# Kernel tuning notes

Hardware: AMD Instinct MI355X
Metric: run time of the kernel (lower is better)

## Reference

```python
import jax, jax.numpy as jnp
import numpy as np

EPS = 1e-8


def setup_inputs() -> dict:
    key = jax.random.key(0)
    ks = jax.random.split(key, 7)
    S, B, E, D, A = 2048, 32, 1024, 1024, 1024
    return {
        "decoder_state": jax.random.normal(ks[0], (B, D), jnp.float32),
        "encoder_states": jax.random.normal(ks[1], (S, B, E), jnp.float32),
        "noise": jax.random.normal(ks[2], (S, B), jnp.float32),
        "W_dec": jax.random.normal(ks[3], (D, A), jnp.float32) * (D ** -0.5),
        "W_enc": jax.random.normal(ks[4], (E, A), jnp.float32) * (E ** -0.5),
        "b": jax.random.normal(ks[5], (A,), jnp.float32) * 0.02,
        "v": jax.random.normal(ks[6], (A,), jnp.float32) * (A ** -0.5),
    }


def reference(decoder_state, encoder_states, noise, W_dec, W_enc, b, v):
    S, B, E = encoder_states.shape
    # Additive (Bahdanau) monotonic energy: e_sb = v . tanh(W_d s + W_e h + b)
    dec_proj = decoder_state @ W_dec                         # [B, A]
    enc_proj = jnp.einsum("sbe,ea->sba", encoder_states, W_enc)  # [S, B, A]
    energy = jnp.einsum("sba,a->sb", jnp.tanh(enc_proj + dec_proj[None] + b), v)
    # p_choose with pre-sigmoid Gaussian noise (noise_avg=0, noise_var=1)
    p_choose = jax.nn.sigmoid(energy + noise)                # [S, B]

    # previous_attention is None -> one-hot at source position 0
    prev_attn = jnp.zeros((S, B), p_choose.dtype).at[0].set(1.0)

    # exclusive cumprod of (1 - p) along src dim
    cp = jnp.cumprod(1.0 - p_choose, axis=0)
    cumprod_one_minus_p = jnp.concatenate(
        [jnp.ones((1, B), p_choose.dtype), cp[:-1]], axis=0)
    denom = jnp.clip(cumprod_one_minus_p, EPS, 1.0)
    alpha = p_choose * cumprod_one_minus_p * jnp.cumsum(prev_attn / denom, axis=0)

    # mass preservation (no padding mask): dump residual mass on last frame
    residual = 1.0 - jnp.clip(jnp.sum(alpha[:-1], axis=0), 0.0, 1.0)
    alpha = alpha.at[-1].set(residual)

    beta = alpha  # hard monotonic attention: beta == alpha
    weighted_context = jnp.einsum("sbe,sb->be", encoder_states, beta)  # [B, E]
    return weighted_context, alpha
```

## Files before the change

### kernel.cpp

```cpp
#include <hip/hip_runtime.h>
#include <hip/hip_fp16.h>

#define S_DIM 2048
#define B_DIM 32
#define E_DIM 1024
#define A_DIM 1024
#define D_DIM 1024
#define M_DIM (S_DIM * B_DIM)

typedef _Float16 f16x8 __attribute__((ext_vector_type(8)));
typedef _Float16 f16x4 __attribute__((ext_vector_type(4)));
typedef float f32x4 __attribute__((ext_vector_type(4)));

#define OFF_ENC 0ull
#define OFF_WT  134217728ull
#define OFF_DP  (OFF_WT + 2097152ull)
#define OFF_EN  (OFF_DP + 131072ull)

__device__ inline void load_lds16(const void* g, void* l) {
    __builtin_amdgcn_global_load_lds((const __attribute__((address_space(1))) void*)g,
                                     (__attribute__((address_space(3))) void*)l, 16, 0, 0);
}

__global__ void convert_enc_kernel(const float4* __restrict__ in, f16x4* __restrict__ out) {
    int idx = blockIdx.x * 256 + threadIdx.x;
    float4 f = in[idx];
    f16x4 o = { (_Float16)f.x, (_Float16)f.y, (_Float16)f.z, (_Float16)f.w };
    out[idx] = o;
}

__global__ void transpose_wenc_kernel(const float* __restrict__ W, _Float16* __restrict__ WT) {
    __shared__ _Float16 tile[32][33];
    int a0 = blockIdx.x * 32, e0 = blockIdx.y * 32;
    int tx = threadIdx.x & 31, ty = threadIdx.x >> 5;
    #pragma unroll
    for (int i = 0; i < 32; i += 8)
        tile[ty + i][tx] = (_Float16)W[(size_t)(e0 + ty + i) * A_DIM + a0 + tx];
    __syncthreads();
    #pragma unroll
    for (int i = 0; i < 32; i += 8)
        WT[(size_t)(a0 + ty + i) * E_DIM + e0 + tx] = tile[tx][ty + i];
}

__global__ void decproj_kernel(const float* __restrict__ dec, const float* __restrict__ Wd,
                               const float* __restrict__ bias, float* __restrict__ dp) {
    int a = blockIdx.x * 256 + threadIdx.x;
    int b = blockIdx.y;
    float acc = bias[a];
    const float* dr = dec + (size_t)b * D_DIM;
    const float* wcol = Wd + a;
    #pragma unroll 8
    for (int d = 0; d < D_DIM; ++d)
        acc += dr[d] * wcol[(size_t)d * A_DIM];
    dp[(size_t)b * A_DIM + a] = acc;
}

__global__ __launch_bounds__(512, 2)
void energy_gemm_kernel(const _Float16* __restrict__ Af, const _Float16* __restrict__ Bt,
                        const float* __restrict__ dp, const float* __restrict__ v,
                        float* __restrict__ energy) {
    __shared__ alignas(16) _Float16 Atile[2][256 * 64];
    __shared__ alignas(16) _Float16 Btile[2][256 * 64];

    const int tid = threadIdx.x;
    const int wid = tid >> 6;
    const int lane = tid & 63;
    const int quad = lane >> 4;
    const int l15 = lane & 15;
    const int l7 = l15 & 7;

    const int bid = blockIdx.x;
    const int xcd = bid & 7;
    const int local = bid >> 3;
    const int m0 = (xcd * 32 + (local >> 2)) * 256;
    const int n0 = (local & 3) * 256;

    const int wm = (wid >> 2) * 128;
    const int wn = (wid & 3) * 64;

    const int lr = lane >> 3;
    const int lcol = ((lane & 7) ^ lr) * 8;
    const int srow = wid * 8;
    const _Float16* Ag = Af + (size_t)(m0 + srow + lr) * E_DIM + lcol;
    const _Float16* Bg = Bt + (size_t)(n0 + srow + lr) * E_DIM + lcol;

#define STAGE(bufi, k0)                                                       \
    {                                                                         \
        _Float16* ad = &Atile[bufi][srow * 64];                               \
        _Float16* bd = &Btile[bufi][srow * 64];                               \
        _Pragma("unroll")                                                     \
        for (int p = 0; p < 4; ++p) {                                         \
            load_lds16(Ag + (size_t)p * 64 * E_DIM + (k0), ad + p * 4096);    \
            load_lds16(Bg + (size_t)p * 64 * E_DIM + (k0), bd + p * 4096);    \
        }                                                                     \
    }

    f32x4 acc[8][4] = {};

    STAGE(0, 0)
    STAGE(1, 64)

    for (int t = 0; t < 16; ++t) {
        const int buf = t & 1;
        if (t == 15) asm volatile("s_waitcnt vmcnt(0)" ::: "memory");
        else         asm volatile("s_waitcnt vmcnt(8)" ::: "memory");
        __builtin_amdgcn_s_barrier();
        asm volatile("" ::: "memory");

        #pragma unroll
        for (int kh = 0; kh < 2; ++kh) {
            f16x8 bf[4];
            #pragma unroll
            for (int j = 0; j < 4; ++j) {
                const int row = wn + j * 16 + l15;
                const int slot = (quad + kh * 4) ^ l7;
                bf[j] = *(const f16x8*)&Btile[buf][row * 64 + slot * 8];
            }
            #pragma unroll
            for (int mh = 0; mh < 2; ++mh) {
                f16x8 af[4];
                #pragma unroll
                for (int i = 0; i < 4; ++i) {
                    const int row = wm + mh * 64 + i * 16 + l15;
                    const int slot = (quad + kh * 4) ^ l7;
                    af[i] = *(const f16x8*)&Atile[buf][row * 64 + slot * 8];
                }
                __builtin_amdgcn_s_setprio(1);
                #pragma unroll
                for (int i = 0; i < 4; ++i)
                    #pragma unroll
                    for (int j = 0; j < 4; ++j)
                        acc[mh * 4 + i][j] = __builtin_amdgcn_mfma_f32_16x16x32_f16(
                            af[i], bf[j], acc[mh * 4 + i][j], 0, 0, 0);
                __builtin_amdgcn_s_setprio(0);
            }
        }

        asm volatile("" ::: "memory");
        __builtin_amdgcn_s_barrier();
        asm volatile("" ::: "memory");
        if (t + 2 < 16) STAGE(buf, (t + 2) * 64)
    }
#undef STAGE

    float vf[4];
    #pragma unroll
    for (int j = 0; j < 4; ++j) vf[j] = v[n0 + wn + j * 16 + l15];

    #pragma unroll
    for (int i = 0; i < 8; ++i) {
        #pragma unroll
        for (int r = 0; r < 4; ++r) {
            int m = m0 + wm + i * 16 + quad * 4 + r;
            int bidx = m & 31;
            float sum = 0.f;
            #pragma unroll
            for (int j = 0; j < 4; ++j) {
                int a = n0 + wn + j * 16 + l15;
                float x = acc[i][j][r] + dp[bidx * A_DIM + a];
                float ex = __expf(2.f * x);
                float th = 1.f - 2.f * __builtin_amdgcn_rcpf(ex + 1.f);
                sum += th * vf[j];
            }
            sum += __shfl_xor(sum, 1);
            sum += __shfl_xor(sum, 2);
            sum += __shfl_xor(sum, 4);
            sum += __shfl_xor(sum, 8);
            if (l15 == 0) atomicAdd(&energy[bidx * S_DIM + (m >> 5)], sum);
        }
    }
}

__global__ void scan_alpha_kernel(const float* __restrict__ energy, const float* __restrict__ noise,
                                  float* __restrict__ alpha) {
    __shared__ float sc[256];
    __shared__ float red[256];
    const int b = blockIdx.x;
    const int t = threadIdx.x;
    float p[8], q[8];
    float prod = 1.f;
    #pragma unroll
    for (int k = 0; k < 8; ++k) {
        int s = t * 8 + k;
        float x = energy[b * S_DIM + s] + noise[s * B_DIM + b];
        p[k] = __builtin_amdgcn_rcpf(1.f + __expf(-x));
        q[k] = __builtin_amdgcn_rcpf(1.f + __expf(x));
        prod *= q[k];
    }
    sc[t] = prod;
    __syncthreads();
    for (int off = 1; off < 256; off <<= 1) {
        float mine = sc[t];
        float other = (t >= off) ? sc[t - off] : 1.f;
        __syncthreads();
        sc[t] = mine * other;
        __syncthreads();
    }
    float run = (t > 0) ? sc[t - 1] : 1.f;
    float lsum = 0.f;
    #pragma unroll
    for (int k = 0; k < 8; ++k) {
        int s = t * 8 + k;
        float al = p[k] * run;
        run *= q[k];
        if (s < S_DIM - 1) { alpha[s * B_DIM + b] = al; lsum += al; }
    }
    red[t] = lsum;
    __syncthreads();
    for (int off = 128; off > 0; off >>= 1) {
        if (t < off) red[t] += red[t + off];
        __syncthreads();
    }
    if (t == 0) {
        float tot = fminf(fmaxf(red[0], 0.f), 1.f);
        alpha[(S_DIM - 1) * B_DIM + b] = 1.f - tot;
    }
}

__global__ void wc_kernel(const _Float16* __restrict__ enc, const float* __restrict__ alpha,
                          float* __restrict__ wc) {
    __shared__ float red[128][8];
    const int b = blockIdx.y;
    const int t = threadIdx.x;
    const int e0 = (t & 127) * 8;
    const int half = t >> 7;
    int s = blockIdx.x * 128 + half;
    float acc[8] = {};
    for (int i = 0; i < 64; ++i, s += 2) {
        float al = alpha[s * B_DIM + b];
        f16x8 r = *(const f16x8*)&enc[((size_t)s * B_DIM + b) * E_DIM + e0];
        #pragma unroll
        for (int k = 0; k < 8; ++k) acc[k] += al * (float)r[k];
    }
    if (half) {
        #pragma unroll
        for (int k = 0; k < 8; ++k) red[t - 128][k] = acc[k];
    }
    __syncthreads();
    if (!half) {
        #pragma unroll
        for (int k = 0; k < 8; ++k)
            atomicAdd(&wc[b * E_DIM + e0 + k], acc[k] + red[t][k]);
    }
}

extern "C" void kernel_launch(void* const* d_in, const int* in_sizes, int n_in,
                              void* d_out, int out_size, void* d_ws, size_t ws_size,
                              hipStream_t stream) {
    const float* dec   = (const float*)d_in[0];
    const float* enc   = (const float*)d_in[1];
    const float* noise = (const float*)d_in[2];
    const float* Wd    = (const float*)d_in[3];
    const float* We    = (const float*)d_in[4];
    const float* bias  = (const float*)d_in[5];
    const float* v     = (const float*)d_in[6];

    char* ws = (char*)d_ws;
    _Float16* encf = (_Float16*)(ws + OFF_ENC);
    _Float16* wtf  = (_Float16*)(ws + OFF_WT);
    float* dp      = (float*)(ws + OFF_DP);
    float* energy  = (float*)(ws + OFF_EN);

    float* wc    = (float*)d_out;
    float* alpha = (float*)d_out + B_DIM * E_DIM;

    (void)hipMemsetAsync(wc, 0, B_DIM * E_DIM * sizeof(float), stream);
    (void)hipMemsetAsync(energy, 0, M_DIM * sizeof(float), stream);

    convert_enc_kernel<<<dim3(M_DIM * E_DIM / 4 / 256), 256, 0, stream>>>((const float4*)enc, (f16x4*)encf);
    transpose_wenc_kernel<<<dim3(32, 32), 256, 0, stream>>>(We, wtf);
    decproj_kernel<<<dim3(4, 32), 256, 0, stream>>>(dec, Wd, bias, dp);
    energy_gemm_kernel<<<dim3(1024), 512, 0, stream>>>(encf, wtf, dp, v, energy);
    scan_alpha_kernel<<<dim3(32), 256, 0, stream>>>(energy, noise, alpha);
    wc_kernel<<<dim3(16, 32), 256, 0, stream>>>(encf, alpha, wc);
}
```

Baseline: 678.9 us.

## Restructure energy GEMM main loop into 4-stage BK=32 pipeline with split A/B staging

```diff
diff --git a/kernel.cpp b/kernel.cpp
--- a/kernel.cpp
+++ b/kernel.cpp
@@ -59,15 +59,14 @@
 void energy_gemm_kernel(const _Float16* __restrict__ Af, const _Float16* __restrict__ Bt,
                         const float* __restrict__ dp, const float* __restrict__ v,
                         float* __restrict__ energy) {
-    __shared__ alignas(16) _Float16 Atile[2][256 * 64];
-    __shared__ alignas(16) _Float16 Btile[2][256 * 64];
+    __shared__ alignas(16) _Float16 As[4][256 * 32];
+    __shared__ alignas(16) _Float16 Bs[4][256 * 32];
 
     const int tid = threadIdx.x;
     const int wid = tid >> 6;
     const int lane = tid & 63;
     const int quad = lane >> 4;
     const int l15 = lane & 15;
-    const int l7 = l15 & 7;
 
     const int bid = blockIdx.x;
     const int xcd = bid & 7;
@@ -78,70 +77,82 @@
     const int wm = (wid >> 2) * 128;
     const int wn = (wid & 3) * 64;
 
-    const int lr = lane >> 3;
-    const int lcol = ((lane & 7) ^ lr) * 8;
-    const int srow = wid * 8;
-    const _Float16* Ag = Af + (size_t)(m0 + srow + lr) * E_DIM + lcol;
-    const _Float16* Bg = Bt + (size_t)(n0 + srow + lr) * E_DIM + lcol;
-
-#define STAGE(bufi, k0)                                                       \
-    {                                                                         \
-        _Float16* ad = &Atile[bufi][srow * 64];                               \
-        _Float16* bd = &Btile[bufi][srow * 64];                               \
-        _Pragma("unroll")                                                     \
-        for (int p = 0; p < 4; ++p) {                                         \
-            load_lds16(Ag + (size_t)p * 64 * E_DIM + (k0), ad + p * 4096);    \
-            load_lds16(Bg + (size_t)p * 64 * E_DIM + (k0), bd + p * 4096);    \
-        }                                                                     \
+    const int lr = lane >> 2;
+    const int lc = (lane & 3) * 8;
+    const _Float16* Ag = Af + (size_t)(m0 + wid * 16 + lr) * E_DIM + lc;
+    const _Float16* Bg = Bt + (size_t)(n0 + wid * 16 + lr) * E_DIM + lc;
+
+#define STAGE_A(u)                                                              \
+    {                                                                           \
+        load_lds16(Ag + (size_t)(u) * 32, &As[(u) & 3][wid * 512]);             \
+        load_lds16(Ag + (size_t)128 * E_DIM + (size_t)(u) * 32,                 \
+                   &As[(u) & 3][(wid + 8) * 512]);                              \
+    }
+#define STAGE_B(u)                                                              \
+    {                                                                           \
+        load_lds16(Bg + (size_t)(u) * 32, &Bs[(u) & 3][wid * 512]);             \
+        load_lds16(Bg + (size_t)128 * E_DIM + (size_t)(u) * 32,                 \
+                   &Bs[(u) & 3][(wid + 8) * 512]);                              \
     }
 
     f32x4 acc[8][4] = {};
 
-    STAGE(0, 0)
-    STAGE(1, 64)
-
-    for (int t = 0; t < 16; ++t) {
-        const int buf = t & 1;
-        if (t == 15) asm volatile("s_waitcnt vmcnt(0)" ::: "memory");
-        else         asm volatile("s_waitcnt vmcnt(8)" ::: "memory");
-        __builtin_amdgcn_s_barrier();
-        asm volatile("" ::: "memory");
-
-        #pragma unroll
-        for (int kh = 0; kh < 2; ++kh) {
-            f16x8 bf[4];
+    STAGE_A(0) STAGE_B(0)
+    STAGE_A(1) STAGE_B(1)
+    STAGE_A(2) STAGE_B(2)
+    asm volatile("s_waitcnt vmcnt(8)" ::: "memory");
+    __builtin_amdgcn_s_barrier();
+    asm volatile("" ::: "memory");
+
+    #pragma unroll
+    for (int t = 0; t < 32; ++t) {
+        const int slot = t & 3;
+        f16x8 af[4], bf[4];
+
+        #pragma unroll
+        for (int j = 0; j < 4; ++j)
+            bf[j] = *(const f16x8*)&Bs[slot][(wn + j * 16 + l15) * 32 + quad * 8];
+        #pragma unroll
+        for (int i = 0; i < 4; ++i)
+            af[i] = *(const f16x8*)&As[slot][(wm + i * 16 + l15) * 32 + quad * 8];
+        if (t < 29) STAGE_A(t + 3)
+        asm volatile("" ::: "memory");
+        __builtin_amdgcn_s_barrier();
+        asm volatile("" ::: "memory");
+        __builtin_amdgcn_s_setprio(1);
+        #pragma unroll
+        for (int i = 0; i < 4; ++i)
             #pragma unroll
-            for (int j = 0; j < 4; ++j) {
-                const int row = wn + j * 16 + l15;
-                const int slot = (quad + kh * 4) ^ l7;
-                bf[j] = *(const f16x8*)&Btile[buf][row * 64 + slot * 8];
-            }
+            for (int j = 0; j < 4; ++j)
+                acc[i][j] = __builtin_amdgcn_mfma_f32_16x16x32_f16(af[i], bf[j], acc[i][j], 0, 0, 0);
+        __builtin_amdgcn_s_setprio(0);
+        asm volatile("" ::: "memory");
+        __builtin_amdgcn_s_barrier();
+        asm volatile("" ::: "memory");
+
+        #pragma unroll
+        for (int i = 0; i < 4; ++i)
+            af[i] = *(const f16x8*)&As[slot][(wm + 64 + i * 16 + l15) * 32 + quad * 8];
+        if (t < 29) STAGE_B(t + 3)
+        asm volatile("" ::: "memory");
+        __builtin_amdgcn_s_barrier();
+        asm volatile("" ::: "memory");
+        __builtin_amdgcn_s_setprio(1);
+        #pragma unroll
+        for (int i = 0; i < 4; ++i)
             #pragma unroll
-            for (int mh = 0; mh < 2; ++mh) {
-                f16x8 af[4];
-                #pragma unroll
-                for (int i = 0; i < 4; ++i) {
-                    const int row = wm + mh * 64 + i * 16 + l15;
-                    const int slot = (quad + kh * 4) ^ l7;
-                    af[i] = *(const f16x8*)&Atile[buf][row * 64 + slot * 8];
-                }
-                __builtin_amdgcn_s_setprio(1);
-                #pragma unroll
-                for (int i = 0; i < 4; ++i)
-                    #pragma unroll
-                    for (int j = 0; j < 4; ++j)
-                        acc[mh * 4 + i][j] = __builtin_amdgcn_mfma_f32_16x16x32_f16(
-                            af[i], bf[j], acc[mh * 4 + i][j], 0, 0, 0);
-                __builtin_amdgcn_s_setprio(0);
-            }
-        }
-
-        asm volatile("" ::: "memory");
-        __builtin_amdgcn_s_barrier();
-        asm volatile("" ::: "memory");
-        if (t + 2 < 16) STAGE(buf, (t + 2) * 64)
-    }
-#undef STAGE
+            for (int j = 0; j < 4; ++j)
+                acc[4 + i][j] = __builtin_amdgcn_mfma_f32_16x16x32_f16(af[i], bf[j], acc[4 + i][j], 0, 0, 0);
+        __builtin_amdgcn_s_setprio(0);
+        if (t <= 28)      asm volatile("s_waitcnt vmcnt(8)" ::: "memory");
+        else if (t == 29) asm volatile("s_waitcnt vmcnt(4)" ::: "memory");
+        else if (t == 30) asm volatile("s_waitcnt vmcnt(0)" ::: "memory");
+        asm volatile("" ::: "memory");
+        __builtin_amdgcn_s_barrier();
+        asm volatile("" ::: "memory");
+    }
+#undef STAGE_A
+#undef STAGE_B
 
     float vf[4];
     #pragma unroll
```

Result: no change. 669.0 us (-1.5%).
